# Optimization experiments

Hardware: AMD Instinct MI355X
Metric: run time of the kernel (lower is better)

Reference implementation:

```python
import jax, jax.numpy as jnp
import numpy as np

B, N, F, D = 8, 2048, 128, 128


def setup_inputs() -> dict:
    key = jax.random.key(0)
    k1, k2, k3 = jax.random.split(key, 3)
    inputs = jax.random.normal(k1, (B, N, F), dtype=jnp.float32)
    adj = jax.random.uniform(k2, (B, N, N), dtype=jnp.float32)  # nonneg weights -> positive degrees
    W_kernel = jax.random.normal(k3, (F, D), dtype=jnp.float32) * (1.0 / np.sqrt(F))
    W_bias = jnp.zeros((D,), dtype=jnp.float32)
    return {"inputs": inputs, "adj": adj, "W_kernel": W_kernel, "W_bias": W_bias}


def _normalize_adjacency(adj):
    # D^{-1/2} A D^{-1/2}: same math as diag-matmul chain, via broadcast scaling
    d = jnp.sum(adj, axis=-1)                      # [B, N]
    d_sqrt_inv = jnp.power(d, -0.5)
    d_sqrt_inv = jnp.where(jnp.isinf(d_sqrt_inv), 0.0, d_sqrt_inv)
    return d_sqrt_inv[..., :, None] * adj * d_sqrt_inv[..., None, :]


def reference(inputs, adj, W_kernel, W_bias):
    adj_norm = _normalize_adjacency(adj)           # [B, N, N]
    feats = inputs @ W_kernel + W_bias             # [B, N, D]
    out = jnp.einsum('bnm,bmd->bnd', adj_norm, feats)
    return jax.nn.relu(out)
```

## Files before the change

### kernel.cpp

```cpp
#include <hip/hip_runtime.h>
#include <hip/hip_bf16.h>
#include <stdint.h>

#define B_ 8
#define N_ 2048
#define F_ 128
#define D_ 128

typedef short bf16x8 __attribute__((ext_vector_type(8)));
typedef float f32x4 __attribute__((ext_vector_type(4)));

__device__ __forceinline__ unsigned short f2bf(float f) {
    unsigned u = __float_as_uint(f);
    u += 0x7fffu + ((u >> 16) & 1u);
    return (unsigned short)(u >> 16);
}

__global__ __launch_bounds__(256) void k_degwt(const float* __restrict__ adj,
                                               const float* __restrict__ W,
                                               float* __restrict__ rs,
                                               unsigned short* __restrict__ Wt) {
    if (blockIdx.x < 4096) {
        const int wave = threadIdx.x >> 6, lane = threadIdx.x & 63;
        const int row = blockIdx.x * 4 + wave;
        const float4* p = (const float4*)(adj + (size_t)row * N_);
        float s = 0.f;
#pragma unroll
        for (int j = 0; j < 8; ++j) {
            float4 v = p[j * 64 + lane];
            s += (v.x + v.y) + (v.z + v.w);
        }
#pragma unroll
        for (int m = 1; m < 64; m <<= 1) s += __shfl_xor(s, m, 64);
        if (lane == 0) rs[row] = (s > 0.f) ? (1.0f / sqrtf(s)) : 0.f;
    } else {
        int c = (blockIdx.x - 4096) * 256 + threadIdx.x;
        int d = c >> 4, f0 = (c & 15) * 8;
        union { bf16x8 v; unsigned short u[8]; } pk;
#pragma unroll
        for (int e = 0; e < 8; ++e) pk.u[e] = f2bf(W[(size_t)(f0 + e) * D_ + d]);
        *(bf16x8*)(Wt + (size_t)d * F_ + f0) = pk.v;
    }
}

__global__ __launch_bounds__(256) void k_feat(const float* __restrict__ x,
                                              const unsigned short* __restrict__ Wt,
                                              const float* __restrict__ bias,
                                              const float* __restrict__ rs,
                                              unsigned short* __restrict__ gt) {
    __shared__ __align__(16) unsigned char sX[64 * 128 * 2];
    __shared__ __align__(16) unsigned char sW[128 * 128 * 2];
    const int t = threadIdx.x;
    const int R0 = blockIdx.x * 64;

#pragma unroll
    for (int j = 0; j < 8; ++j) {
        int c = j * 256 + t;
        unsigned L = (unsigned)c * 16u;
        unsigned lg = L ^ (((L >> 8) & 7u) << 4);
        const unsigned char* src = (const unsigned char*)Wt + lg;
        __builtin_amdgcn_global_load_lds(
            (const __attribute__((address_space(1))) void*)src,
            (__attribute__((address_space(3))) void*)(sW + L), 16, 0, 0);
    }
#pragma unroll
    for (int j = 0; j < 4; ++j) {
        int c = j * 256 + t;
        int row = c >> 4, sub = c & 15;
        const float4* src = (const float4*)(x + (size_t)(R0 + row) * F_ + sub * 8);
        float4 v0 = src[0], v1 = src[1];
        union { bf16x8 v; unsigned short u[8]; } pk;
        pk.u[0] = f2bf(v0.x); pk.u[1] = f2bf(v0.y); pk.u[2] = f2bf(v0.z); pk.u[3] = f2bf(v0.w);
        pk.u[4] = f2bf(v1.x); pk.u[5] = f2bf(v1.y); pk.u[6] = f2bf(v1.z); pk.u[7] = f2bf(v1.w);
        unsigned byte = (unsigned)(row * 256 + sub * 16);
        byte ^= ((byte >> 8) & 7u) << 4;
        *(bf16x8*)(sX + byte) = pk.v;
    }
    __syncthreads();

    const int w = t >> 6, l = t & 63, lr = l & 15, lh = l >> 4;
    f32x4 acc[8];
#pragma unroll
    for (int j = 0; j < 8; ++j) acc[j] = (f32x4){0.f, 0.f, 0.f, 0.f};

#pragma unroll
    for (int ks = 0; ks < 4; ++ks) {
        unsigned abyte = (unsigned)((w * 16 + lr) * 256 + lh * 16 + ks * 64);
        abyte ^= ((abyte >> 8) & 7u) << 4;
        bf16x8 a = *(const bf16x8*)(sX + abyte);
#pragma unroll
        for (int j = 0; j < 8; ++j) {
            unsigned bbyte = (unsigned)((j * 16 + lr) * 256 + lh * 16 + ks * 64);
            bbyte ^= ((bbyte >> 8) & 7u) << 4;
            bf16x8 bb = *(const bf16x8*)(sW + bbyte);
            acc[j] = __builtin_amdgcn_mfma_f32_16x16x32_bf16(a, bb, acc[j], 0, 0, 0);
        }
    }

    const int m0 = R0 + w * 16 + lh * 4;
    float4 r4 = *(const float4*)(rs + m0);
    float rr[4] = {r4.x, r4.y, r4.z, r4.w};
#pragma unroll
    for (int j = 0; j < 8; ++j) {
        int d = j * 16 + lr;
        float bv = bias[d];
#pragma unroll
        for (int r = 0; r < 4; ++r) {
            int m = m0 + r;
            int b = m >> 11, n = m & (N_ - 1);
            gt[((size_t)b * D_ + d) * N_ + n] = f2bf((acc[j][r] + bv) * rr[r]);
        }
    }
}

__global__ __launch_bounds__(512) void k_gcn(const float* __restrict__ adj,
                                             const unsigned short* __restrict__ gt,
                                             const float* __restrict__ rs,
                                             float* __restrict__ out) {
    __shared__ __align__(16) unsigned char sA[2][32 * 128 * 2];
    __shared__ __align__(16) unsigned char sB[2][128 * 128 * 2];

    unsigned bid = blockIdx.x;
    unsigned wg = (bid & 7u) * 64u + (bid >> 3);
    const int b = (int)(wg >> 6);
    const int R0 = (int)(wg & 63u) * 32;

    const float* adjB = adj + (size_t)b * N_ * N_ + (size_t)R0 * N_;
    const unsigned short* gtB = gt + (size_t)b * D_ * N_;
    const float* rsB = rs + (size_t)b * N_;

    const int t = threadIdx.x;
    const int w = t >> 6, l = t & 63, lr = l & 15, lh = l >> 4;
    const int kg = w >> 2, cg = w & 3;

    auto stage = [&](int bufidx, int k0) {
        unsigned char* sBb = sB[bufidx];
#pragma unroll
        for (int i = 0; i < 4; ++i) {
            int c = i * 512 + t;
            unsigned L = (unsigned)c * 16u;
            unsigned lg = L ^ (((L >> 8) & 7u) << 4);
            int d = (int)(lg >> 8);
            int mloc = (int)(lg & 255u) >> 1;
            const unsigned short* g = gtB + (size_t)d * N_ + k0 + mloc;
            __builtin_amdgcn_global_load_lds(
                (const __attribute__((address_space(1))) void*)g,
                (__attribute__((address_space(3))) void*)(sBb + L), 16, 0, 0);
        }
        {
            int row = t >> 4, sub = t & 15;
            const float4* src = (const float4*)(adjB + (size_t)row * N_ + k0 + sub * 8);
            float4 v0 = src[0], v1 = src[1];
            union { bf16x8 v; unsigned short u[8]; } pk;
            pk.u[0] = f2bf(v0.x); pk.u[1] = f2bf(v0.y);
            pk.u[2] = f2bf(v0.z); pk.u[3] = f2bf(v0.w);
            pk.u[4] = f2bf(v1.x); pk.u[5] = f2bf(v1.y);
            pk.u[6] = f2bf(v1.z); pk.u[7] = f2bf(v1.w);
            unsigned byte = (unsigned)(row * 256 + sub * 16);
            byte ^= ((byte >> 8) & 7u) << 4;
            *(bf16x8*)(sA[bufidx] + byte) = pk.v;
        }
    };

    f32x4 acc[2][2];
#pragma unroll
    for (int i = 0; i < 2; ++i)
#pragma unroll
        for (int jn = 0; jn < 2; ++jn) acc[i][jn] = (f32x4){0.f, 0.f, 0.f, 0.f};

    stage(0, 0);
    __syncthreads();

    const int NITER = N_ / 128;
    for (int it = 0; it < NITER; ++it) {
        int cur = it & 1;
        if (it + 1 < NITER) stage(cur ^ 1, (it + 1) * 128);

        const unsigned char* pA = sA[cur];
        const unsigned char* pB = sB[cur];
#pragma unroll
        for (int kk2 = 0; kk2 < 2; ++kk2) {
            const int kk = kg * 2 + kk2;
            bf16x8 a[2], bb[2];
#pragma unroll
            for (int i = 0; i < 2; ++i) {
                unsigned byte = (unsigned)((i * 16 + lr) * 256 + lh * 16 + kk * 64);
                byte ^= ((byte >> 8) & 7u) << 4;
                a[i] = *(const bf16x8*)(pA + byte);
            }
#pragma unroll
            for (int jn = 0; jn < 2; ++jn) {
                int d = cg * 32 + jn * 16 + lr;
                unsigned byte = (unsigned)(d * 256 + lh * 16 + kk * 64);
                byte ^= ((byte >> 8) & 7u) << 4;
                bb[jn] = *(const bf16x8*)(pB + byte);
            }
#pragma unroll
            for (int i = 0; i < 2; ++i)
#pragma unroll
                for (int jn = 0; jn < 2; ++jn)
                    acc[i][jn] = __builtin_amdgcn_mfma_f32_16x16x32_bf16(a[i], bb[jn], acc[i][jn], 0, 0, 0);
        }
        __syncthreads();
    }

    float* sO = (float*)sA;
    if (kg == 1) {
#pragma unroll
        for (int i = 0; i < 2; ++i)
#pragma unroll
            for (int jn = 0; jn < 2; ++jn)
#pragma unroll
                for (int r = 0; r < 4; ++r) {
                    int rowl = i * 16 + lh * 4 + r;
                    int d = cg * 32 + jn * 16 + lr;
                    sO[rowl * 128 + d] = acc[i][jn][r];
                }
    }
    __syncthreads();
    if (kg == 0) {
#pragma unroll
        for (int i = 0; i < 2; ++i) {
            float4 r4 = *(const float4*)(rsB + R0 + i * 16 + lh * 4);
            float rr[4] = {r4.x, r4.y, r4.z, r4.w};
#pragma unroll
            for (int r = 0; r < 4; ++r) {
                int rowl = i * 16 + lh * 4 + r;
#pragma unroll
                for (int jn = 0; jn < 2; ++jn) {
                    int d = cg * 32 + jn * 16 + lr;
                    float v = (acc[i][jn][r] + sO[rowl * 128 + d]) * rr[r];
                    out[((size_t)(b * N_ + R0 + rowl)) * D_ + d] = fmaxf(v, 0.f);
                }
            }
        }
    }
}

extern "C" void kernel_launch(void* const* d_in, const int* in_sizes, int n_in,
                              void* d_out, int out_size, void* d_ws, size_t ws_size,
                              hipStream_t stream) {
    const float* inputs = (const float*)d_in[0];
    const float* adj    = (const float*)d_in[1];
    const float* Wk     = (const float*)d_in[2];
    const float* Wb     = (const float*)d_in[3];
    float* out = (float*)d_out;

    float* rs = (float*)d_ws;
    unsigned short* gt = (unsigned short*)((char*)d_ws + 65536);
    unsigned short* Wt = (unsigned short*)((char*)d_ws + 65536 + (size_t)B_ * D_ * N_ * 2);

    k_degwt<<<4096 + 8, 256, 0, stream>>>(adj, Wk, rs, Wt);
    k_feat <<<(B_ * N_) / 64, 256, 0, stream>>>(inputs, Wt, Wb, rs, gt);
    k_gcn  <<<B_ * (N_ / 32), 512, 0, stream>>>(adj, gt, rs, out);
}
```

Measured before the change: 55.64 us.

## Prefetch adjacency into registers and defer bf16 conversion with manual waitcnt

The main GCN kernel now issues the next tile's adjacency float loads into registers alongside the async gt-to-LDS loads. It converts the current tile to bf16 with packed v_cvt_pk_bf16_f32 instructions and writes it to LDS just before the compute barrier. Load addresses are precomputed once, and __syncthreads is replaced with explicit vmcnt/lgkmcnt waits plus s_barrier. The intent is to hide the adjacency load latency behind compute instead of stalling inside the stage function. The cost is more live registers and fragile hand-counted wait counts.

```diff
diff --git a/kernel.cpp b/kernel.cpp
--- a/kernel.cpp
+++ b/kernel.cpp
@@ -133,32 +133,28 @@
     const int w = t >> 6, l = t & 63, lr = l & 15, lh = l >> 4;
     const int kg = w >> 2, cg = w & 3;
 
-    auto stage = [&](int bufidx, int k0) {
-        unsigned char* sBb = sB[bufidx];
+    const float* aSrc = adjB + (size_t)(t >> 4) * N_ + (t & 15) * 8;
+    unsigned aL = (unsigned)((t >> 4) * 256 + (t & 15) * 16);
+    aL ^= ((aL >> 8) & 7u) << 4;
+
+    const unsigned short* bSrc[4];
+    unsigned bL[4];
+#pragma unroll
+    for (int i = 0; i < 4; ++i) {
+        unsigned c = (unsigned)(i * 512 + t);
+        unsigned L = c * 16u;
+        unsigned lg = L ^ (((L >> 8) & 7u) << 4);
+        bL[i] = L;
+        bSrc[i] = gtB + (size_t)(lg >> 8) * N_ + ((lg & 255u) >> 1);
+    }
+
+    auto issueB = [&](int buf, int k0) {
+        unsigned char* pB = sB[buf];
 #pragma unroll
         for (int i = 0; i < 4; ++i) {
-            int c = i * 512 + t;
-            unsigned L = (unsigned)c * 16u;
-            unsigned lg = L ^ (((L >> 8) & 7u) << 4);
-            int d = (int)(lg >> 8);
-            int mloc = (int)(lg & 255u) >> 1;
-            const unsigned short* g = gtB + (size_t)d * N_ + k0 + mloc;
             __builtin_amdgcn_global_load_lds(
-                (const __attribute__((address_space(1))) void*)g,
-                (__attribute__((address_space(3))) void*)(sBb + L), 16, 0, 0);
-        }
-        {
-            int row = t >> 4, sub = t & 15;
-            const float4* src = (const float4*)(adjB + (size_t)row * N_ + k0 + sub * 8);
-            float4 v0 = src[0], v1 = src[1];
-            union { bf16x8 v; unsigned short u[8]; } pk;
-            pk.u[0] = f2bf(v0.x); pk.u[1] = f2bf(v0.y);
-            pk.u[2] = f2bf(v0.z); pk.u[3] = f2bf(v0.w);
-            pk.u[4] = f2bf(v1.x); pk.u[5] = f2bf(v1.y);
-            pk.u[6] = f2bf(v1.z); pk.u[7] = f2bf(v1.w);
-            unsigned byte = (unsigned)(row * 256 + sub * 16);
-            byte ^= ((byte >> 8) & 7u) << 4;
-            *(bf16x8*)(sA[bufidx] + byte) = pk.v;
+                (const __attribute__((address_space(1))) void*)(bSrc[i] + k0),
+                (__attribute__((address_space(3))) void*)(pB + bL[i]), 16, 0, 0);
         }
     };
 
@@ -168,13 +164,38 @@
 #pragma unroll
         for (int jn = 0; jn < 2; ++jn) acc[i][jn] = (f32x4){0.f, 0.f, 0.f, 0.f};
 
-    stage(0, 0);
-    __syncthreads();
+    issueB(0, 0);
+    float4 a0 = *(const float4*)(aSrc);
+    float4 a1 = *(const float4*)(aSrc + 4);
 
     const int NITER = N_ / 128;
     for (int it = 0; it < NITER; ++it) {
-        int cur = it & 1;
-        if (it + 1 < NITER) stage(cur ^ 1, (it + 1) * 128);
+        const int cur = it & 1;
+        float4 n0 = a0, n1 = a1;
+        if (it + 1 < NITER) {
+            issueB(cur ^ 1, (it + 1) * 128);
+            const float* s = aSrc + (it + 1) * 128;
+            n0 = *(const float4*)(s);
+            n1 = *(const float4*)(s + 4);
+            asm volatile("s_waitcnt vmcnt(6)" ::: "memory");
+        } else {
+            asm volatile("s_waitcnt vmcnt(0)" ::: "memory");
+        }
+        __builtin_amdgcn_sched_barrier(0);
+
+        {
+            unsigned u0, u1, u2, u3;
+            asm("v_cvt_pk_bf16_f32 %0, %1, %2" : "=v"(u0) : "v"(a0.x), "v"(a0.y));
+            asm("v_cvt_pk_bf16_f32 %0, %1, %2" : "=v"(u1) : "v"(a0.z), "v"(a0.w));
+            asm("v_cvt_pk_bf16_f32 %0, %1, %2" : "=v"(u2) : "v"(a1.x), "v"(a1.y));
+            asm("v_cvt_pk_bf16_f32 %0, %1, %2" : "=v"(u3) : "v"(a1.z), "v"(a1.w));
+            union { unsigned u[4]; bf16x8 v; } pk;
+            pk.u[0] = u0; pk.u[1] = u1; pk.u[2] = u2; pk.u[3] = u3;
+            *(bf16x8*)(sA[cur] + aL) = pk.v;
+        }
+        asm volatile("s_waitcnt lgkmcnt(0)" ::: "memory");
+        __builtin_amdgcn_sched_barrier(0);
+        __builtin_amdgcn_s_barrier();
 
         const unsigned char* pA = sA[cur];
         const unsigned char* pB = sB[cur];
@@ -201,7 +222,9 @@
                 for (int jn = 0; jn < 2; ++jn)
                     acc[i][jn] = __builtin_amdgcn_mfma_f32_16x16x32_bf16(a[i], bb[jn], acc[i][jn], 0, 0, 0);
         }
-        __syncthreads();
+        __builtin_amdgcn_s_barrier();
+
+        a0 = n0; a1 = n1;
     }
 
     float* sO = (float*)sA;
@@ -251,6 +274,6 @@
     unsigned short* Wt = (unsigned short*)((char*)d_ws + 65536 + (size_t)B_ * D_ * N_ * 2);
 
     k_degwt<<<4096 + 8, 256, 0, stream>>>(adj, Wk, rs, Wt);
-    k_feat <<<(B_ * N_) / 64, 256, 0, stream>>>(inputs, Wt, Wb, rs, gt);
+    k_feat <<<(B_ * N_) / 64, 256, 0, stream>>>(inputs, Wk == nullptr ? nullptr : Wt, Wb, rs, gt);
     k_gcn  <<<B_ * (N_ / 32), 512, 0, stream>>>(adj, gt, rs, out);
 }
```

After: 55.40 us. No clear change (-0.4%).

## Rewrite GCN aggregation kernel with 4-stage software pipeline and 64-row tiles

Applied to the files above, without the earlier changes.

The main aggregation kernel now uses 64-row output tiles with K-step 64 and a 4-deep LDS ring buffer. Explicit vmcnt/lgkmcnt waits and barriers overlap global loads of the adjacency and feature tiles with MFMA work. The previous split-K reduction through shared memory is gone, and adjacency conversion to bf16 now uses packed cvt instructions. The grid shrinks to 256 blocks, one per CU, which lowers launch count but relies on hand-tuned wait counts being correct.

```diff
diff --git a/kernel.cpp b/kernel.cpp
--- a/kernel.cpp
+++ b/kernel.cpp
@@ -113,54 +113,102 @@
     }
 }
 
+#define BUFSZ (24 * 1024)
+#define VM(n) asm volatile("s_waitcnt vmcnt(" #n ")" ::: "memory")
+#define LGKM0 asm volatile("s_waitcnt lgkmcnt(0)" ::: "memory")
+#define SCHED __builtin_amdgcn_sched_barrier(0)
+#define BAR __builtin_amdgcn_s_barrier()
+
 __global__ __launch_bounds__(512) void k_gcn(const float* __restrict__ adj,
                                              const unsigned short* __restrict__ gt,
                                              const float* __restrict__ rs,
                                              float* __restrict__ out) {
-    __shared__ __align__(16) unsigned char sA[2][32 * 128 * 2];
-    __shared__ __align__(16) unsigned char sB[2][128 * 128 * 2];
-
-    unsigned bid = blockIdx.x;
-    unsigned wg = (bid & 7u) * 64u + (bid >> 3);
-    const int b = (int)(wg >> 6);
-    const int R0 = (int)(wg & 63u) * 32;
-
-    const float* adjB = adj + (size_t)b * N_ * N_ + (size_t)R0 * N_;
+    __shared__ __align__(16) unsigned char sBuf[4 * BUFSZ];
+
+    const int bid = blockIdx.x;
+    const int b = bid & 7;
+    const int R0 = (bid >> 3) * 64;
+
+    const float* adjB = adj + (size_t)(b * N_ + R0) * N_;
     const unsigned short* gtB = gt + (size_t)b * D_ * N_;
     const float* rsB = rs + (size_t)b * N_;
 
     const int t = threadIdx.x;
     const int w = t >> 6, l = t & 63, lr = l & 15, lh = l >> 4;
-    const int kg = w >> 2, cg = w & 3;
-
-    auto stage = [&](int bufidx, int k0) {
-        unsigned char* sBb = sB[bufidx];
-#pragma unroll
-        for (int i = 0; i < 4; ++i) {
-            int c = i * 512 + t;
-            unsigned L = (unsigned)c * 16u;
-            unsigned lg = L ^ (((L >> 8) & 7u) << 4);
-            int d = (int)(lg >> 8);
-            int mloc = (int)(lg & 255u) >> 1;
-            const unsigned short* g = gtB + (size_t)d * N_ + k0 + mloc;
-            __builtin_amdgcn_global_load_lds(
-                (const __attribute__((address_space(1))) void*)g,
-                (__attribute__((address_space(3))) void*)(sBb + L), 16, 0, 0);
-        }
-        {
-            int row = t >> 4, sub = t & 15;
-            const float4* src = (const float4*)(adjB + (size_t)row * N_ + k0 + sub * 8);
-            float4 v0 = src[0], v1 = src[1];
-            union { bf16x8 v; unsigned short u[8]; } pk;
-            pk.u[0] = f2bf(v0.x); pk.u[1] = f2bf(v0.y);
-            pk.u[2] = f2bf(v0.z); pk.u[3] = f2bf(v0.w);
-            pk.u[4] = f2bf(v1.x); pk.u[5] = f2bf(v1.y);
-            pk.u[6] = f2bf(v1.z); pk.u[7] = f2bf(v1.w);
-            unsigned byte = (unsigned)(row * 256 + sub * 16);
-            byte ^= ((byte >> 8) & 7u) << 4;
-            *(bf16x8*)(sA[bufidx] + byte) = pk.v;
-        }
-    };
+    const int wr = w >> 2, wc = w & 3;
+
+    const float* aSrc = adjB + (size_t)(t >> 3) * N_ + (t & 7) * 8;
+    const unsigned aRow = (unsigned)(t >> 3);
+    unsigned aL = aRow * 128u + (unsigned)((t & 7) * 16);
+    aL ^= ((aRow & 7u) << 4) ^ ((aRow & 8u) << 3);
+
+    const unsigned short* bSrc0;
+    const unsigned short* bSrc1;
+    unsigned bL0, bL1;
+    {
+        unsigned c0 = (unsigned)t, c1 = (unsigned)(512 + t);
+        unsigned L0 = c0 * 16u, L1 = c1 * 16u;
+        unsigned d0 = L0 >> 7, d1 = L1 >> 7;
+        unsigned w0 = (L0 & 127u) ^ ((d0 & 7u) << 4) ^ ((d0 & 8u) << 3);
+        unsigned w1 = (L1 & 127u) ^ ((d1 & 7u) << 4) ^ ((d1 & 8u) << 3);
+        bSrc0 = gtB + (size_t)d0 * N_ + (w0 >> 1);
+        bSrc1 = gtB + (size_t)d1 * N_ + (w1 >> 1);
+        bL0 = 8192u + L0; bL1 = 8192u + L1;
+    }
+
+    f32x4 aR0a, aR0b, aR1a, aR1b, aR2a, aR2b, aR3a, aR3b;
+
+#define STAGE(J, S) do {                                                          \
+    unsigned char* pBuf = sBuf + ((unsigned)(J) & 3u) * BUFSZ;                    \
+    __builtin_amdgcn_global_load_lds(                                             \
+        (const __attribute__((address_space(1))) void*)(bSrc0 + (J) * 64),       \
+        (__attribute__((address_space(3))) void*)(pBuf + bL0), 16, 0, 0);        \
+    __builtin_amdgcn_global_load_lds(                                             \
+        (const __attribute__((address_space(1))) void*)(bSrc1 + (J) * 64),       \
+        (__attribute__((address_space(3))) void*)(pBuf + bL1), 16, 0, 0);        \
+    aR##S##a = *(const f32x4*)(aSrc + (J) * 64);                                  \
+    aR##S##b = *(const f32x4*)(aSrc + (J) * 64 + 4);                              \
+} while (0)
+
+#define CVTW(J, S) do {                                                           \
+    unsigned u0, u1, u2, u3;                                                      \
+    asm("v_cvt_pk_bf16_f32 %0, %1, %2" : "=v"(u0) : "v"(aR##S##a[0]), "v"(aR##S##a[1])); \
+    asm("v_cvt_pk_bf16_f32 %0, %1, %2" : "=v"(u1) : "v"(aR##S##a[2]), "v"(aR##S##a[3])); \
+    asm("v_cvt_pk_bf16_f32 %0, %1, %2" : "=v"(u2) : "v"(aR##S##b[0]), "v"(aR##S##b[1])); \
+    asm("v_cvt_pk_bf16_f32 %0, %1, %2" : "=v"(u3) : "v"(aR##S##b[2]), "v"(aR##S##b[3])); \
+    union { unsigned uu[4]; bf16x8 v; } pk;                                       \
+    pk.uu[0] = u0; pk.uu[1] = u1; pk.uu[2] = u2; pk.uu[3] = u3;                   \
+    *(bf16x8*)(sBuf + ((unsigned)(J) & 3u) * BUFSZ + aL) = pk.v;                  \
+} while (0)
+
+#define MFMA_IT(IT) do {                                                          \
+    const unsigned char* pA = sBuf + ((unsigned)(IT) & 3u) * BUFSZ;               \
+    const unsigned char* pB = pA + 8192;                                          \
+    _Pragma("unroll")                                                             \
+    for (int kk = 0; kk < 2; ++kk) {                                              \
+        bf16x8 a_[2], b_[2];                                                      \
+        _Pragma("unroll")                                                         \
+        for (int i = 0; i < 2; ++i) {                                             \
+            unsigned row = (unsigned)(wr * 32 + i * 16 + lr);                     \
+            unsigned byte = row * 128u + (unsigned)(kk * 64 + lh * 16);           \
+            byte ^= ((row & 7u) << 4) ^ ((row & 8u) << 3);                        \
+            a_[i] = *(const bf16x8*)(pA + byte);                                  \
+        }                                                                         \
+        _Pragma("unroll")                                                         \
+        for (int jn = 0; jn < 2; ++jn) {                                          \
+            unsigned d = (unsigned)(wc * 32 + jn * 16 + lr);                      \
+            unsigned byte = d * 128u + (unsigned)(kk * 64 + lh * 16);             \
+            byte ^= ((d & 7u) << 4) ^ ((d & 8u) << 3);                            \
+            b_[jn] = *(const bf16x8*)(pB + byte);                                 \
+        }                                                                         \
+        _Pragma("unroll")                                                         \
+        for (int i = 0; i < 2; ++i)                                               \
+            _Pragma("unroll")                                                     \
+            for (int jn = 0; jn < 2; ++jn)                                        \
+                acc[i][jn] = __builtin_amdgcn_mfma_f32_16x16x32_bf16(             \
+                    a_[i], b_[jn], acc[i][jn], 0, 0, 0);                          \
+    }                                                                             \
+} while (0)
 
     f32x4 acc[2][2];
 #pragma unroll
@@ -168,70 +216,56 @@
 #pragma unroll
         for (int jn = 0; jn < 2; ++jn) acc[i][jn] = (f32x4){0.f, 0.f, 0.f, 0.f};
 
-    stage(0, 0);
-    __syncthreads();
-
-    const int NITER = N_ / 128;
-    for (int it = 0; it < NITER; ++it) {
-        int cur = it & 1;
-        if (it + 1 < NITER) stage(cur ^ 1, (it + 1) * 128);
-
-        const unsigned char* pA = sA[cur];
-        const unsigned char* pB = sB[cur];
-#pragma unroll
-        for (int kk2 = 0; kk2 < 2; ++kk2) {
-            const int kk = kg * 2 + kk2;
-            bf16x8 a[2], bb[2];
-#pragma unroll
-            for (int i = 0; i < 2; ++i) {
-                unsigned byte = (unsigned)((i * 16 + lr) * 256 + lh * 16 + kk * 64);
-                byte ^= ((byte >> 8) & 7u) << 4;
-                a[i] = *(const bf16x8*)(pA + byte);
-            }
+    STAGE(0, 0);
+    STAGE(1, 1);
+    STAGE(2, 2);
+    VM(8);
+    SCHED;
+    CVTW(0, 0);
+    LGKM0; SCHED;
+
+    for (int it4 = 0; it4 < 7; ++it4) {
+        const int itb = it4 * 4;
+        STAGE(itb + 3, 3); VM(12); SCHED; BAR;
+        MFMA_IT(0);
+        VM(8); SCHED; CVTW(itb + 1, 1); LGKM0; SCHED; BAR;
+        STAGE(itb + 4, 0); VM(12); SCHED; BAR;
+        MFMA_IT(1);
+        VM(8); SCHED; CVTW(itb + 2, 2); LGKM0; SCHED; BAR;
+        STAGE(itb + 5, 1); VM(12); SCHED; BAR;
+        MFMA_IT(2);
+        VM(8); SCHED; CVTW(itb + 3, 3); LGKM0; SCHED; BAR;
+        STAGE(itb + 6, 2); VM(12); SCHED; BAR;
+        MFMA_IT(3);
+        VM(8); SCHED; CVTW(itb + 4, 0); LGKM0; SCHED; BAR;
+    }
+    STAGE(31, 3); VM(12); SCHED; BAR;
+    MFMA_IT(28);
+    VM(8); SCHED; CVTW(29, 1); LGKM0; SCHED; BAR;
+
+    VM(8); SCHED; BAR;
+    MFMA_IT(29);
+    VM(4); SCHED; CVTW(30, 2); LGKM0; SCHED; BAR;
+
+    VM(4); SCHED; BAR;
+    MFMA_IT(30);
+    VM(0); SCHED; CVTW(31, 3); LGKM0; SCHED; BAR;
+
+    BAR;
+    MFMA_IT(31);
+
+#pragma unroll
+    for (int i = 0; i < 2; ++i) {
+        float4 r4 = *(const float4*)(rsB + R0 + wr * 32 + i * 16 + lh * 4);
+        float rr[4] = {r4.x, r4.y, r4.z, r4.w};
+#pragma unroll
+        for (int r = 0; r < 4; ++r) {
+            int rowl = wr * 32 + i * 16 + lh * 4 + r;
 #pragma unroll
             for (int jn = 0; jn < 2; ++jn) {
-                int d = cg * 32 + jn * 16 + lr;
-                unsigned byte = (unsigned)(d * 256 + lh * 16 + kk * 64);
-                byte ^= ((byte >> 8) & 7u) << 4;
-                bb[jn] = *(const bf16x8*)(pB + byte);
-            }
-#pragma unroll
-            for (int i = 0; i < 2; ++i)
-#pragma unroll
-                for (int jn = 0; jn < 2; ++jn)
-                    acc[i][jn] = __builtin_amdgcn_mfma_f32_16x16x32_bf16(a[i], bb[jn], acc[i][jn], 0, 0, 0);
-        }
-        __syncthreads();
-    }
-
-    float* sO = (float*)sA;
-    if (kg == 1) {
-#pragma unroll
-        for (int i = 0; i < 2; ++i)
-#pragma unroll
-            for (int jn = 0; jn < 2; ++jn)
-#pragma unroll
-                for (int r = 0; r < 4; ++r) {
-                    int rowl = i * 16 + lh * 4 + r;
-                    int d = cg * 32 + jn * 16 + lr;
-                    sO[rowl * 128 + d] = acc[i][jn][r];
-                }
-    }
-    __syncthreads();
-    if (kg == 0) {
-#pragma unroll
-        for (int i = 0; i < 2; ++i) {
-            float4 r4 = *(const float4*)(rsB + R0 + i * 16 + lh * 4);
-            float rr[4] = {r4.x, r4.y, r4.z, r4.w};
-#pragma unroll
-            for (int r = 0; r < 4; ++r) {
-                int rowl = i * 16 + lh * 4 + r;
-#pragma unroll
-                for (int jn = 0; jn < 2; ++jn) {
-                    int d = cg * 32 + jn * 16 + lr;
-                    float v = (acc[i][jn][r] + sO[rowl * 128 + d]) * rr[r];
-                    out[((size_t)(b * N_ + R0 + rowl)) * D_ + d] = fmaxf(v, 0.f);
-                }
+                int d = wc * 32 + jn * 16 + lr;
+                float v = acc[i][jn][r] * rr[r];
+                out[((size_t)(b * N_ + R0 + rowl)) * D_ + d] = fmaxf(v, 0.f);
             }
         }
     }
@@ -246,11 +280,12 @@
     const float* Wb     = (const float*)d_in[3];
     float* out = (float*)d_out;
 
-    float* rs = (float*)d_ws;
-    unsigned short* gt = (unsigned short*)((char*)d_ws + 65536);
-    unsigned short* Wt = (unsigned short*)((char*)d_ws + 65536 + (size_t)B_ * D_ * N_ * 2);
+    char* ws = (char*)d_ws;
+    float* rs          = (float*)ws;
+    unsigned short* gt = (unsigned short*)(ws + (1 << 20));
+    unsigned short* Wt = (unsigned short*)(ws + (6 << 20));
 
     k_degwt<<<4096 + 8, 256, 0, stream>>>(adj, Wk, rs, Wt);
     k_feat <<<(B_ * N_) / 64, 256, 0, stream>>>(inputs, Wt, Wb, rs, gt);
-    k_gcn  <<<B_ * (N_ / 32), 512, 0, stream>>>(adj, gt, rs, out);
-}
+    k_gcn  <<<256, 512, 0, stream>>>(adj, gt, rs, out);
+}
```

Result: faster. 54.46 us (-2.1%).
